# Kernel tuning notes

Hardware: AMD Instinct MI355X
Metric: run time of the kernel (lower is better)

The kernel has to match this reference:

```python
import jax, jax.numpy as jnp
import numpy as np

# Idealized internal coordinates for N, CA, C, CB (order matches original dict iteration)
INTERNAL_COORD = np.array([
    [1.460091, 0.0, 0.0],            # N
    [0.0, 0.0, 0.0],                  # CA
    [-0.56431316, 1.41695817, 0.0],   # C
    [-0.52426314, -0.76611338, 1.20561194],  # CB
], dtype=np.float32)

B, L = 32, 65536


def setup_inputs() -> dict:
    key = jax.random.key(0)
    k1, k2 = jax.random.split(key)
    return {
        "translation": jax.random.normal(k1, (B, L, 3), dtype=jnp.float32),
        "quaternion": jax.random.normal(k2, (B, L, 4), dtype=jnp.float32),
    }


def _quat_to_rot(q):
    # q: (..., 4) -> R: (..., 3, 3)
    r, i, j, k = q[..., 0], q[..., 1], q[..., 2], q[..., 3]
    row0 = jnp.stack([1 - 2 * (j * j + k * k), 2 * (i * j - k * r), 2 * (i * k + j * r)], axis=-1)
    row1 = jnp.stack([2 * (i * j + k * r), 1 - 2 * (i * i + k * k), 2 * (j * k - i * r)], axis=-1)
    row2 = jnp.stack([2 * (i * k - j * r), 2 * (j * k + i * r), 1 - 2 * (i * i + j * j)], axis=-1)
    return jnp.stack([row0, row1, row2], axis=-2)


def reference(translation, quaternion):
    # normalize(): center translation over residue dim, unit-normalize quaternion
    t = translation - jnp.mean(translation, axis=1, keepdims=True)          # (B,L,3)
    q = quaternion / (jnp.linalg.norm(quaternion, axis=-1, keepdims=True) + 1e-6)
    R = _quat_to_rot(q)                                                     # (B,L,3,3)
    P = jnp.asarray(INTERNAL_COORD)                                         # (4,3) atoms N,CA,C,CB
    # rotate each fixed atom coord and translate: (B,L,4,3)
    coords = jnp.einsum('blij,aj->blai', R, P) + t[:, :, None, :]
    return coords  # coords[..., 0, :] = N, 1 = CA, 2 = C, 3 = CB
```

## Files before the change

### kernel.cpp

```cpp
#include <hip/hip_runtime.h>


#define BB 32
#define LL 65536
#define S1_BLOCKS 512
#define S1_TPB 512
#define S1_GROUPS_PER_BLOCK 1024
#define PPB 16

#define P_TPB 1024
#define RES_PER_BLOCK 1024
#define POSE_BLOCKS ((BB * LL) / RES_PER_BLOCK)

typedef float f32x4 __attribute__((ext_vector_type(4)));

__global__ __launch_bounds__(S1_TPB) void partial_sums_kernel(
    const f32x4* __restrict__ trans4, float* __restrict__ partials) {
    const int bid = blockIdx.x;
    const int tid = threadIdx.x;

    float s0 = 0.f, s1 = 0.f, s2 = 0.f;
#pragma unroll
    for (int it = 0; it < 2; ++it) {
        const size_t m = ((size_t)bid * S1_GROUPS_PER_BLOCK + it * S1_TPB + tid) * 3;
        const f32x4 a = trans4[m + 0];
        const f32x4 c = trans4[m + 1];
        const f32x4 d = trans4[m + 2];
        s0 += a.x + a.w + c.z + d.y;
        s1 += a.y + c.x + c.w + d.z;
        s2 += a.z + c.y + d.x + d.w;
    }

#pragma unroll
    for (int off = 32; off > 0; off >>= 1) {
        s0 += __shfl_down(s0, off);
        s1 += __shfl_down(s1, off);
        s2 += __shfl_down(s2, off);
    }
    __shared__ float red[8][3];
    const int wave = tid >> 6;
    if ((tid & 63) == 0) { red[wave][0] = s0; red[wave][1] = s1; red[wave][2] = s2; }
    __syncthreads();
    if (tid < 3) {
        float s = 0.f;
#pragma unroll
        for (int w = 0; w < 8; ++w) s += red[w][tid];
        partials[bid * 3 + tid] = s;
    }
}

__global__ __launch_bounds__(P_TPB) void pose_kernel(
    const f32x4* __restrict__ trans4, const f32x4* __restrict__ quat4,
    const float* __restrict__ partials, f32x4* __restrict__ out4) {
    __shared__ f32x4 stage[RES_PER_BLOCK * 3];
    __shared__ float mean[3];

    const int tid = threadIdx.x;
    const int b = blockIdx.x >> 6;
    const size_t r0 = (size_t)blockIdx.x * RES_PER_BLOCK;

    const f32x4 q4 = quat4[r0 + tid];
    if (tid < RES_PER_BLOCK * 3 / 4)
        stage[tid] = trans4[(size_t)blockIdx.x * (RES_PER_BLOCK * 3 / 4) + tid];
    if (tid < 3) {
        float s = 0.f;
#pragma unroll
        for (int p = 0; p < PPB; ++p) s += partials[(b * PPB + p) * 3 + tid];
        mean[tid] = s * (1.0f / (float)LL);
    }
    __syncthreads();

    const float mx = mean[0], my = mean[1], mz = mean[2];
    const float* sf = (const float*)stage;
    const float tx = sf[tid * 3 + 0] - mx;
    const float ty = sf[tid * 3 + 1] - my;
    const float tz = sf[tid * 3 + 2] - mz;

    float r = q4.x, i = q4.y, j = q4.z, k = q4.w;
    const float inv = 1.0f / (sqrtf(r * r + i * i + j * j + k * k) + 1e-6f);
    r *= inv; i *= inv; j *= inv; k *= inv;

    const float R00 = 1.f - 2.f * (j * j + k * k);
    const float R01 = 2.f * (i * j - k * r);
    const float R02 = 2.f * (i * k + j * r);
    const float R10 = 2.f * (i * j + k * r);
    const float R11 = 1.f - 2.f * (i * i + k * k);
    const float R12 = 2.f * (j * k - i * r);
    const float R20 = 2.f * (i * k - j * r);
    const float R21 = 2.f * (j * k + i * r);
    const float R22 = 1.f - 2.f * (i * i + j * j);

    const float Nx = 1.460091f;
    const float Cx = -0.56431316f, Cy = 1.41695817f;
    const float Bx = -0.52426314f, By = -0.76611338f, Bz = 1.20561194f;

    const float N0 = R00 * Nx + tx, N1 = R10 * Nx + ty, N2 = R20 * Nx + tz;
    const float C0 = R00 * Cx + R01 * Cy + tx;
    const float C1 = R10 * Cx + R11 * Cy + ty;
    const float C2 = R20 * Cx + R21 * Cy + tz;
    const float B0 = R00 * Bx + R01 * By + R02 * Bz + tx;
    const float B1 = R10 * Bx + R11 * By + R12 * Bz + ty;
    const float B2 = R20 * Bx + R21 * By + R22 * Bz + tz;

    __syncthreads();
    stage[tid * 3 + 0] = (f32x4){N0, N1, N2, tx};
    stage[tid * 3 + 1] = (f32x4){ty, tz, C0, C1};
    stage[tid * 3 + 2] = (f32x4){C2, B0, B1, B2};
    __syncthreads();

    const size_t ob = r0 * 3;
    __builtin_nontemporal_store(stage[0 * P_TPB + tid], &out4[ob + 0 * P_TPB + tid]);
    __builtin_nontemporal_store(stage[1 * P_TPB + tid], &out4[ob + 1 * P_TPB + tid]);
    __builtin_nontemporal_store(stage[2 * P_TPB + tid], &out4[ob + 2 * P_TPB + tid]);
}

extern "C" void kernel_launch(void* const* d_in, const int* in_sizes, int n_in,
                              void* d_out, int out_size, void* d_ws, size_t ws_size,
                              hipStream_t stream) {
    const f32x4* trans4 = (const f32x4*)d_in[0];
    const f32x4* quat4 = (const f32x4*)d_in[1];
    f32x4* out4 = (f32x4*)d_out;

    float* partials = (float*)d_ws;

    partial_sums_kernel<<<S1_BLOCKS, S1_TPB, 0, stream>>>(trans4, partials);
    pose_kernel<<<POSE_BLOCKS, P_TPB, 0, stream>>>(trans4, quat4, partials, out4);
}
```

Measured before the change: 38.72 us.

## Restructure pose kernel into 256-thread blocks looping over prefetched chunks

Pose kernel now uses 256 threads per block, each block still covering 1024 residues but in four sequential chunks of 256. The quaternion and translation loads for the next chunk are issued before the current chunk is computed, with a double-buffered shared translation tile, so global loads overlap compute and stores. This cuts shared memory per block and raises the number of resident blocks, at the cost of two barriers per chunk and less parallelism per block.

```diff
diff --git a/kernel.cpp b/kernel.cpp
--- a/kernel.cpp
+++ b/kernel.cpp
@@ -8,9 +8,10 @@
 #define S1_GROUPS_PER_BLOCK 1024
 #define PPB 16
 
-#define P_TPB 1024
-#define RES_PER_BLOCK 1024
-#define POSE_BLOCKS ((BB * LL) / RES_PER_BLOCK)
+#define P_TPB 256
+#define CHUNKS 4
+#define RES_PER_POSE_BLOCK 1024
+#define POSE_BLOCKS ((BB * LL) / RES_PER_POSE_BLOCK)
 
 typedef float f32x4 __attribute__((ext_vector_type(4)));
 
@@ -52,16 +53,18 @@
 __global__ __launch_bounds__(P_TPB) void pose_kernel(
     const f32x4* __restrict__ trans4, const f32x4* __restrict__ quat4,
     const float* __restrict__ partials, f32x4* __restrict__ out4) {
-    __shared__ f32x4 stage[RES_PER_BLOCK * 3];
+    __shared__ f32x4 strans[2][192];
+    __shared__ f32x4 sout[768];
     __shared__ float mean[3];
 
     const int tid = threadIdx.x;
-    const int b = blockIdx.x >> 6;
-    const size_t r0 = (size_t)blockIdx.x * RES_PER_BLOCK;
+    const int bid = blockIdx.x;
+    const int b = bid >> 6;
+    const size_t r0 = (size_t)bid * RES_PER_POSE_BLOCK;
+    const size_t tbase = (size_t)bid * (RES_PER_POSE_BLOCK * 3 / 4);
 
-    const f32x4 q4 = quat4[r0 + tid];
-    if (tid < RES_PER_BLOCK * 3 / 4)
-        stage[tid] = trans4[(size_t)blockIdx.x * (RES_PER_BLOCK * 3 / 4) + tid];
+    f32x4 qv = quat4[r0 + tid];
+    if (tid < 192) strans[0][tid] = trans4[tbase + tid];
     if (tid < 3) {
         float s = 0.f;
 #pragma unroll
@@ -69,49 +72,63 @@
         mean[tid] = s * (1.0f / (float)LL);
     }
     __syncthreads();
-
     const float mx = mean[0], my = mean[1], mz = mean[2];
-    const float* sf = (const float*)stage;
-    const float tx = sf[tid * 3 + 0] - mx;
-    const float ty = sf[tid * 3 + 1] - my;
-    const float tz = sf[tid * 3 + 2] - mz;
-
-    float r = q4.x, i = q4.y, j = q4.z, k = q4.w;
-    const float inv = 1.0f / (sqrtf(r * r + i * i + j * j + k * k) + 1e-6f);
-    r *= inv; i *= inv; j *= inv; k *= inv;
-
-    const float R00 = 1.f - 2.f * (j * j + k * k);
-    const float R01 = 2.f * (i * j - k * r);
-    const float R02 = 2.f * (i * k + j * r);
-    const float R10 = 2.f * (i * j + k * r);
-    const float R11 = 1.f - 2.f * (i * i + k * k);
-    const float R12 = 2.f * (j * k - i * r);
-    const float R20 = 2.f * (i * k - j * r);
-    const float R21 = 2.f * (j * k + i * r);
-    const float R22 = 1.f - 2.f * (i * i + j * j);
 
     const float Nx = 1.460091f;
     const float Cx = -0.56431316f, Cy = 1.41695817f;
     const float Bx = -0.52426314f, By = -0.76611338f, Bz = 1.20561194f;
 
-    const float N0 = R00 * Nx + tx, N1 = R10 * Nx + ty, N2 = R20 * Nx + tz;
-    const float C0 = R00 * Cx + R01 * Cy + tx;
-    const float C1 = R10 * Cx + R11 * Cy + ty;
-    const float C2 = R20 * Cx + R21 * Cy + tz;
-    const float B0 = R00 * Bx + R01 * By + R02 * Bz + tx;
-    const float B1 = R10 * Bx + R11 * By + R12 * Bz + ty;
-    const float B2 = R20 * Bx + R21 * By + R22 * Bz + tz;
+    f32x4 qn, tn;
+#pragma unroll
+    for (int ch = 0; ch < CHUNKS; ++ch) {
+        if (ch < CHUNKS - 1) {
+            qn = quat4[r0 + (ch + 1) * P_TPB + tid];
+            if (tid < 192) tn = trans4[tbase + (ch + 1) * 192 + tid];
+        }
 
-    __syncthreads();
-    stage[tid * 3 + 0] = (f32x4){N0, N1, N2, tx};
-    stage[tid * 3 + 1] = (f32x4){ty, tz, C0, C1};
-    stage[tid * 3 + 2] = (f32x4){C2, B0, B1, B2};
-    __syncthreads();
+        const float* sf = (const float*)strans[ch & 1];
+        const float tx = sf[tid * 3 + 0] - mx;
+        const float ty = sf[tid * 3 + 1] - my;
+        const float tz = sf[tid * 3 + 2] - mz;
 
-    const size_t ob = r0 * 3;
-    __builtin_nontemporal_store(stage[0 * P_TPB + tid], &out4[ob + 0 * P_TPB + tid]);
-    __builtin_nontemporal_store(stage[1 * P_TPB + tid], &out4[ob + 1 * P_TPB + tid]);
-    __builtin_nontemporal_store(stage[2 * P_TPB + tid], &out4[ob + 2 * P_TPB + tid]);
+        float r = qv.x, i = qv.y, j = qv.z, k = qv.w;
+        const float inv = 1.0f / (sqrtf(r * r + i * i + j * j + k * k) + 1e-6f);
+        r *= inv; i *= inv; j *= inv; k *= inv;
+
+        const float R00 = 1.f - 2.f * (j * j + k * k);
+        const float R01 = 2.f * (i * j - k * r);
+        const float R02 = 2.f * (i * k + j * r);
+        const float R10 = 2.f * (i * j + k * r);
+        const float R11 = 1.f - 2.f * (i * i + k * k);
+        const float R12 = 2.f * (j * k - i * r);
+        const float R20 = 2.f * (i * k - j * r);
+        const float R21 = 2.f * (j * k + i * r);
+        const float R22 = 1.f - 2.f * (i * i + j * j);
+
+        const float N0 = R00 * Nx + tx, N1 = R10 * Nx + ty, N2 = R20 * Nx + tz;
+        const float C0 = R00 * Cx + R01 * Cy + tx;
+        const float C1 = R10 * Cx + R11 * Cy + ty;
+        const float C2 = R20 * Cx + R21 * Cy + tz;
+        const float B0 = R00 * Bx + R01 * By + R02 * Bz + tx;
+        const float B1 = R10 * Bx + R11 * By + R12 * Bz + ty;
+        const float B2 = R20 * Bx + R21 * By + R22 * Bz + tz;
+
+        sout[tid * 3 + 0] = (f32x4){N0, N1, N2, tx};
+        sout[tid * 3 + 1] = (f32x4){ty, tz, C0, C1};
+        sout[tid * 3 + 2] = (f32x4){C2, B0, B1, B2};
+        __syncthreads();
+
+        const size_t ob = (size_t)bid * (RES_PER_POSE_BLOCK * 3) + (size_t)ch * 768;
+        __builtin_nontemporal_store(sout[0 * P_TPB + tid], &out4[ob + 0 * P_TPB + tid]);
+        __builtin_nontemporal_store(sout[1 * P_TPB + tid], &out4[ob + 1 * P_TPB + tid]);
+        __builtin_nontemporal_store(sout[2 * P_TPB + tid], &out4[ob + 2 * P_TPB + tid]);
+
+        if (ch < CHUNKS - 1) {
+            if (tid < 192) strans[(ch + 1) & 1][tid] = tn;
+            qv = qn;
+        }
+        __syncthreads();
+    }
 }
 
 extern "C" void kernel_launch(void* const* d_in, const int* in_sizes, int n_in,
```

New measurement: 33.90 us. 12.4% less time.
